# Kernel optimization log

Measured on AMD Instinct MI355X. Metric: run time of the kernel, lower is better.

The kernel has to match this reference:

```python
import math
import jax, jax.numpy as jnp
import numpy as np

B, T, C = 2, 2048, 1024
N_HEAD = 16
HEAD_DIM = C // N_HEAD

def setup_inputs() -> dict:
    key = jax.random.key(0)
    kx, kq, kk, kv, kp = jax.random.split(key, 5)
    s = 1.0 / math.sqrt(C)
    return {
        "x": jax.random.normal(kx, (B, T, C), dtype=jnp.float32),
        "Wq": jax.random.normal(kq, (C, C), dtype=jnp.float32) * s,
        "Wk": jax.random.normal(kk, (C, C), dtype=jnp.float32) * s,
        "Wv": jax.random.normal(kv, (C, C), dtype=jnp.float32) * s,
        "Wproj": jax.random.normal(kp, (C, C), dtype=jnp.float32) * s,
    }

def reference(x, Wq, Wk, Wv, Wproj):
    b, t, c = x.shape
    # nn.Linear(no bias): x @ W.T ; weights stored [out, in]
    def heads(w):
        return (x @ w.T).reshape(b, t, N_HEAD, HEAD_DIM).transpose(0, 2, 1, 3)  # [B,H,T,D]
    q, k, v = heads(Wq), heads(Wk), heads(Wv)
    att = jnp.einsum('bhqd,bhkd->bhqk', q, k) / math.sqrt(HEAD_DIM)  # [B,H,T,T]
    causal = jnp.tril(jnp.ones((t, t), dtype=bool))
    att = jnp.where(causal, att, -jnp.inf)
    att = jax.nn.softmax(att, axis=-1)
    y = jnp.einsum('bhqk,bhkd->bhqd', att, v)           # [B,H,T,D]
    y = y.transpose(0, 2, 1, 3).reshape(b, t, c)        # [B,T,C]
    return y @ Wproj.T
```

## Files before the change

### kernel.cpp

```cpp
#include <hip/hip_runtime.h>
#include <stdint.h>

typedef uint16_t u16;
typedef uint32_t u32;
typedef __attribute__((ext_vector_type(8))) _Float16 f16x8;
typedef __attribute__((ext_vector_type(4))) float f32x4;
typedef __attribute__((ext_vector_type(2))) uint32_t u32x2;

#define NB 2
#define NT 2048
#define NC 1024
#define NH 16
#define ND 64
#define NM (NB*NT)
#define LOG2E 1.44269504088896340736f
#define PSTRIDE 4608

__device__ __forceinline__ u16 f2h(float f) {
  _Float16 h = (_Float16)f;
  return __builtin_bit_cast(u16, h);
}

__global__ __launch_bounds__(256) void cvt_kernel(const float* __restrict__ src,
                                                  u16* __restrict__ dst, int n4) {
  int i = blockIdx.x * 256 + threadIdx.x;
  if (i >= n4) return;
  float4 v = ((const float4*)src)[i];
  ushort4 o;
  o.x = f2h(v.x); o.y = f2h(v.y); o.z = f2h(v.z); o.w = f2h(v.w);
  ((ushort4*)dst)[i] = o;
}

__global__ __launch_bounds__(256) void cvtw_kernel(const float* __restrict__ w0,
                                                   const float* __restrict__ w1,
                                                   const float* __restrict__ w2,
                                                   const float* __restrict__ w3,
                                                   u16* __restrict__ dst) {
  int i = blockIdx.x * 256 + threadIdx.x;
  int which = i >> 18;
  const float* src = (which == 0) ? w0 : (which == 1) ? w1 : (which == 2) ? w2 : w3;
  int j = i & 262143;
  float4 v = ((const float4*)src)[j];
  ushort4 o;
  o.x = f2h(v.x); o.y = f2h(v.y); o.z = f2h(v.z); o.w = f2h(v.w);
  ((ushort4*)dst)[i] = o;
}

__device__ __forceinline__ void gload16(const void* g, void* l) {
  __builtin_amdgcn_global_load_lds(
      (const __attribute__((address_space(1))) void*)g,
      (__attribute__((address_space(3))) void*)l, 16, 0, 0);
}

template<int EPI>
__global__ __launch_bounds__(256) void gemm_bt(const u16* __restrict__ A,
                                               const u16* __restrict__ Bw,
                                               int K, int N,
                                               u16* __restrict__ oq, u16* __restrict__ okk,
                                               u16* __restrict__ ovt,
                                               float* __restrict__ of) {
  __shared__ __align__(16) u16 SH[4*128*64];
  u16* Al = SH;
  u16* Bl = SH + 2*128*64;
  const int tid = threadIdx.x, lane = tid & 63, wid = tid >> 6;
  const int g = lane >> 4, qq = lane & 15;
  const int wm = wid >> 1, wn = wid & 1;
  const int m0 = blockIdx.y * 128, n0 = blockIdx.x * 128;
  const int srow = lane >> 3;
  const int scol8 = (lane & 7) ^ srow;

  f32x4 acc[4][4] = {};
  const int nk = K >> 6;

  #pragma unroll
  for (int pp = 0; pp < 4; ++pp) {
    int r = wid*32 + pp*8;
    gload16(A  + (size_t)(m0 + r + srow)*K + scol8*8, &Al[r*64]);
    gload16(Bw + (size_t)(n0 + r + srow)*K + scol8*8, &Bl[r*64]);
  }

  for (int kt = 0; kt < nk; ++kt) {
    const int cur = kt & 1;
    __syncthreads();
    if (kt + 1 < nk) {
      const int k1 = (kt + 1) << 6;
      #pragma unroll
      for (int pp = 0; pp < 4; ++pp) {
        int r = wid*32 + pp*8;
        gload16(A  + (size_t)(m0 + r + srow)*K + k1 + scol8*8, &Al[(cur^1)*8192 + r*64]);
        gload16(Bw + (size_t)(n0 + r + srow)*K + k1 + scol8*8, &Bl[(cur^1)*8192 + r*64]);
      }
    }
    #pragma unroll
    for (int kk = 0; kk < 2; ++kk) {
      f16x8 af[4], bfr[4];
      #pragma unroll
      for (int mt = 0; mt < 4; ++mt) {
        int row = wm*64 + mt*16 + qq;
        af[mt] = *(const f16x8*)&Al[cur*8192 + row*64 + (((kk*4 + g) ^ (qq & 7))*8)];
      }
      #pragma unroll
      for (int nt = 0; nt < 4; ++nt) {
        int row = wn*64 + nt*16 + qq;
        bfr[nt] = *(const f16x8*)&Bl[cur*8192 + row*64 + (((kk*4 + g) ^ (qq & 7))*8)];
      }
      #pragma unroll
      for (int mt = 0; mt < 4; ++mt)
        #pragma unroll
        for (int nt = 0; nt < 4; ++nt)
          acc[mt][nt] = __builtin_amdgcn_mfma_f32_16x16x32_f16(af[mt], bfr[nt], acc[mt][nt], 0, 0, 0);
    }
  }

  if (EPI == 0) {
    __syncthreads();
    u16* reg = SH + wid*4096;
    const int sel = n0 >> 10;
    const int h = ((n0 & 1023) >> 6) + wn;
    const int bq = m0 >> 11;

    if (sel < 2) {
      const float scale = (sel == 0) ? 0.125f*LOG2E : 1.0f;
      #pragma unroll
      for (int mt = 0; mt < 4; ++mt)
        #pragma unroll
        for (int r = 0; r < 4; ++r) {
          int mloc = mt*16 + g*4 + r;
          #pragma unroll
          for (int nt = 0; nt < 4; ++nt) {
            int d = nt*16 + qq;
            reg[mloc*64 + (d ^ (g << 4))] = f2h(acc[mt][nt][r] * scale);
          }
        }
      u16* dst = (sel == 0) ? oq : okk;
      const int slot = lane & 7;
      #pragma unroll
      for (int i = 0; i < 8; ++i) {
        int row = i*8 + (lane >> 3);
        int physslot = slot ^ (((row >> 2) & 3) << 1);
        f16x8 vvv = *(const f16x8*)&reg[row*64 + physslot*8];
        int m = m0 + wm*64 + row;
        int t = m & (NT-1);
        *(f16x8*)(dst + (((size_t)(bq*NH + h)*NT + t)*ND) + slot*8) = vvv;
      }
    } else {
      #pragma unroll
      for (int nt = 0; nt < 4; ++nt) {
        int d = nt*16 + qq;
        int f = (d & 7) << 3;
        #pragma unroll
        for (int mt = 0; mt < 4; ++mt)
          #pragma unroll
          for (int rp = 0; rp < 2; ++rp) {
            int r = rp*2;
            int mloc = mt*16 + g*4 + r;
            u32 pk = (u32)f2h(acc[mt][nt][r]) | ((u32)f2h(acc[mt][nt][r+1]) << 16);
            *(u32*)&reg[d*64 + (mloc ^ f)] = pk;
          }
      }
      const int slot = lane & 7;
      const int t0 = m0 + wm*64;
      #pragma unroll
      for (int i = 0; i < 8; ++i) {
        int d = i*8 + (lane >> 3);
        int physslot = slot ^ (d & 7);
        f16x8 vvv = *(const f16x8*)&reg[d*64 + physslot*8];
        int t = (t0 & (NT-1)) + slot*8;
        *(f16x8*)(ovt + ((size_t)(bq*NH + h)*ND + d)*NT + t) = vvv;
      }
    }
  } else {
    #pragma unroll
    for (int mt = 0; mt < 4; ++mt)
      #pragma unroll
      for (int r = 0; r < 4; ++r) {
        int m = m0 + wm*64 + mt*16 + g*4 + r;
        #pragma unroll
        for (int nt = 0; nt < 4; ++nt) {
          int n = n0 + wn*64 + nt*16 + qq;
          of[(size_t)m*N + n] = acc[mt][nt][r];
        }
      }
  }
}

#define IT(q,s,c,m) ((u32)(q) | ((u32)(s)<<8) | ((u32)(c)<<16) | ((u32)(m)<<24))
__global__ __launch_bounds__(256) void attn_kernel(const u16* __restrict__ q,
                                                   const u16* __restrict__ k,
                                                   const u16* __restrict__ vt,
                                                   u16* __restrict__ y,
                                                   u16* __restrict__ part) {
  static const u32 items[48] = {
    IT(15,0,16,0), IT(30,0,16,1), IT(31,0,16,1), IT(31,16,16,2),
    IT(14,0,15,0), IT(28,0,15,1), IT(29,0,15,1), IT(29,15,15,2), IT(30,16,15,2),
    IT(13,0,14,0), IT(26,0,14,1), IT(27,0,14,1), IT(27,14,14,2), IT(28,15,14,2),
    IT(12,0,13,0), IT(24,0,13,1), IT(25,0,13,1), IT(25,13,13,2), IT(26,14,13,2),
    IT(11,0,12,0), IT(22,0,12,1), IT(23,0,12,1), IT(23,12,12,2), IT(24,13,12,2),
    IT(10,0,11,0), IT(20,0,11,1), IT(21,0,11,1), IT(21,11,11,2), IT(22,12,11,2),
    IT( 9,0,10,0), IT(18,0,10,1), IT(19,0,10,1), IT(19,10,10,2), IT(20,11,10,2),
    IT( 8,0, 9,0), IT(16,0, 9,1), IT(17,0, 9,1), IT(17, 9, 9,2), IT(18,10, 9,2),
    IT( 7,0, 8,0), IT(16,9, 8,2),
    IT( 6,0, 7,0), IT( 5,0, 6,0), IT( 4,0, 5,0), IT( 3,0, 4,0),
    IT( 2,0, 3,0), IT( 1,0, 2,0), IT( 0,0, 1,0)
  };
  __shared__ __align__(16) u16 Kl[2][64*64];
  __shared__ __align__(16) u16 Vl[2][64*64];
  __shared__ __align__(16) u16 Pl[4*16*64];
  const int tid = threadIdx.x, lane = tid & 63, wid = tid >> 6;
  const int g = lane >> 4, qq = lane & 15;
  const int bh = blockIdx.x;
  const u32 it = items[blockIdx.y];
  const int qtile = it & 255;
  const int ks = (it >> 8) & 255;
  const int kc = (it >> 16) & 255;
  const int mode = it >> 24;
  const int qs = qtile * 64;
  const u16* qp = q  + (size_t)bh*NT*ND;
  const u16* kp = k  + (size_t)bh*NT*ND;
  const u16* vp = vt + (size_t)bh*ND*NT;
  const int b = bh >> 4, h = bh & 15;
  const int srow = lane >> 3;
  const int scol8 = (lane & 7) ^ (srow & 7);
  u16* pl = &Pl[wid*1024];
  u32* plw = (u32*)pl;

  f16x8 aq[2];
  {
    int t = qs + wid*16 + qq;
    #pragma unroll
    for (int c = 0; c < 2; ++c)
      aq[c] = *(const f16x8*)(qp + (size_t)t*ND + c*32 + 8*g);
  }

  f16x8 vones;
  #pragma unroll
  for (int i = 0; i < 8; ++i) vones[i] = (_Float16)1.0f;

  f32x4 accO[4] = {};
  f32x4 accS = {};
  float m_run = -1e30f;

  #pragma unroll
  for (int pp = 0; pp < 2; ++pp) {
    int issue = wid*2 + pp;
    int row = issue*8 + srow;
    gload16(kp + (size_t)(ks*64 + row)*ND + scol8*8, &Kl[0][issue*512]);
    gload16(vp + (size_t)row*NT + ks*64 + scol8*8, &Vl[0][issue*512]);
  }

  for (int kt = ks; kt < ks + kc; ++kt) {
    const int kvs = kt*64;
    const int cur = (kt - ks) & 1;
    __syncthreads();

    if (kt + 1 < ks + kc) {
      const int kvs2 = kvs + 64;
      #pragma unroll
      for (int pp = 0; pp < 2; ++pp) {
        int issue = wid*2 + pp;
        int row = issue*8 + srow;
        gload16(kp + (size_t)(kvs2 + row)*ND + scol8*8, &Kl[cur^1][issue*512]);
        gload16(vp + (size_t)row*NT + kvs2 + scol8*8, &Vl[cur^1][issue*512]);
      }
    }

    f32x4 sacc[4] = {};
    __builtin_amdgcn_s_setprio(1);
    #pragma unroll
    for (int c = 0; c < 2; ++c) {
      #pragma unroll
      for (int nt = 0; nt < 4; ++nt) {
        int row = nt*16 + qq;
        int col = (c*32 + 8*g) ^ ((row & 7) << 3);
        f16x8 kb = *(const f16x8*)&Kl[cur][row*64 + col];
        sacc[nt] = __builtin_amdgcn_mfma_f32_16x16x32_f16(kb, aq[c], sacc[nt], 0, 0, 0);
      }
    }
    __builtin_amdgcn_s_setprio(0);

    if (kvs + 63 > qs + wid*16) {
      int qg = qs + wid*16 + qq;
      #pragma unroll
      for (int nt = 0; nt < 4; ++nt)
        #pragma unroll
        for (int r = 0; r < 4; ++r)
          if (kvs + nt*16 + g*4 + r > qg) sacc[nt][r] = -1e30f;
    }

    float m0a = fmaxf(fmaxf(sacc[0][0], sacc[0][1]), fmaxf(sacc[0][2], sacc[0][3]));
    float m1a = fmaxf(fmaxf(sacc[1][0], sacc[1][1]), fmaxf(sacc[1][2], sacc[1][3]));
    float m2a = fmaxf(fmaxf(sacc[2][0], sacc[2][1]), fmaxf(sacc[2][2], sacc[2][3]));
    float m3a = fmaxf(fmaxf(sacc[3][0], sacc[3][1]), fmaxf(sacc[3][2], sacc[3][3]));
    float mloc = fmaxf(fmaxf(m0a, m1a), fmaxf(m2a, m3a));

    const bool defer = __all(mloc <= m_run + 8.f);
    float mnew;
    if (defer) {
      mnew = m_run;
    } else {
      float mf = fmaxf(mloc, __shfl_xor(mloc, 16));
      mf = fmaxf(mf, __shfl_xor(mf, 32));
      mnew = fmaxf(m_run, mf);
      float a = exp2f(m_run - mnew);
      m_run = mnew;
      #pragma unroll
      for (int r = 0; r < 4; ++r) {
        float ar = __shfl(a, (lane & 48) + g*4 + r);
        #pragma unroll
        for (int nt = 0; nt < 4; ++nt) accO[nt][r] *= ar;
        accS[r] *= ar;
      }
    }

    #pragma unroll
    for (int nt = 0; nt < 4; ++nt) {
      float p0 = exp2f(sacc[nt][0] - mnew);
      float p1 = exp2f(sacc[nt][1] - mnew);
      float p2 = exp2f(sacc[nt][2] - mnew);
      float p3 = exp2f(sacc[nt][3] - mnew);
      u32 pk0 = __builtin_bit_cast(u32, __builtin_amdgcn_cvt_pkrtz(p0, p1));
      u32 pk1 = __builtin_bit_cast(u32, __builtin_amdgcn_cvt_pkrtz(p2, p3));
      int kv0 = nt*16 + g*4;
      u32x2 pr; pr.x = pk0; pr.y = pk1;
      *(u32x2*)&plw[(qq*64 + (kv0 ^ ((qq & 7) << 3))) >> 1] = pr;
    }

    __builtin_amdgcn_s_setprio(1);
    #pragma unroll
    for (int c = 0; c < 2; ++c) {
      f16x8 pa = *(const f16x8*)&pl[qq*64 + ((c*32 + 8*g) ^ ((qq & 7) << 3))];
      accS = __builtin_amdgcn_mfma_f32_16x16x32_f16(pa, vones, accS, 0, 0, 0);
      #pragma unroll
      for (int nt = 0; nt < 4; ++nt) {
        int vrow = nt*16 + qq;
        int vcol = (c*32 + 8*g) ^ ((vrow & 7) << 3);
        f16x8 vb = *(const f16x8*)&Vl[cur][vrow*64 + vcol];
        accO[nt] = __builtin_amdgcn_mfma_f32_16x16x32_f16(pa, vb, accO[nt], 0, 0, 0);
      }
    }
    __builtin_amdgcn_s_setprio(0);
  }

  if (mode == 0) {
    #pragma unroll
    for (int r = 0; r < 4; ++r) {
      float invr = 1.0f / accS[r];
      int t = qs + wid*16 + g*4 + r;
      #pragma unroll
      for (int nt = 0; nt < 4; ++nt) {
        int d = nt*16 + qq;
        y[((size_t)(b*NT + t))*NC + h*ND + d] = f2h(accO[nt][r] * invr);
      }
    }
  } else {
    const int slot = ((bh << 4) + (qtile - 16))*2 + (mode - 1);
    u16* pp = part + (size_t)slot * PSTRIDE;
    float* hd = (float*)(pp + 4096);
    #pragma unroll
    for (int r = 0; r < 4; ++r) {
      int rloc = wid*16 + g*4 + r;
      float l = accS[r];
      float invr = 1.0f / l;
      float mr = __shfl(m_run, (lane & 48) + g*4 + r);
      #pragma unroll
      for (int nt = 0; nt < 4; ++nt) {
        int d = nt*16 + qq;
        pp[rloc*64 + d] = f2h(accO[nt][r] * invr);
      }
      if (qq == 0) { hd[rloc] = mr; hd[64 + rloc] = l; }
    }
  }
}

__global__ __launch_bounds__(256) void combine_kernel(const u16* __restrict__ part,
                                                      u16* __restrict__ y) {
  const int jj = blockIdx.x;
  const int bh = blockIdx.y;
  const int b = bh >> 4, h = bh & 15;
  const u16* p0 = part + (size_t)(((bh << 4) + jj)*2) * PSTRIDE;
  const u16* p1 = p0 + PSTRIDE;
  const float* h0 = (const float*)(p0 + 4096);
  const float* h1 = (const float*)(p1 + 4096);
  const int tid = threadIdx.x;
  const int d0 = (tid & 7) * 8;
  #pragma unroll
  for (int i = 0; i < 2; ++i) {
    int r = (tid >> 3) + 32*i;
    float m1 = h0[r], l1 = h0[64 + r];
    float m2 = h1[r], l2 = h1[64 + r];
    float mm = fmaxf(m1, m2);
    float w1 = exp2f(m1 - mm) * l1, w2 = exp2f(m2 - mm) * l2;
    float inv = 1.0f / (w1 + w2);
    float a1 = w1 * inv, a2 = w2 * inv;
    f16x8 o1 = *(const f16x8*)&p0[r*64 + d0];
    f16x8 o2 = *(const f16x8*)&p1[r*64 + d0];
    f16x8 out;
    #pragma unroll
    for (int e = 0; e < 8; ++e)
      out[e] = (_Float16)(a1 * (float)o1[e] + a2 * (float)o2[e]);
    int t = (16 + jj)*64 + r;
    *(f16x8*)(y + ((size_t)(b*NT + t))*NC + h*ND + d0) = out;
  }
}

extern "C" void kernel_launch(void* const* d_in, const int* in_sizes, int n_in,
                              void* d_out, int out_size, void* d_ws, size_t ws_size,
                              hipStream_t stream) {
  const float* x  = (const float*)d_in[0];
  const float* Wq = (const float*)d_in[1];
  const float* Wk = (const float*)d_in[2];
  const float* Wv = (const float*)d_in[3];
  const float* Wp = (const float*)d_in[4];

  u16* xb   = (u16*)d_ws;
  u16* wqkv = xb   + (size_t)NM*NC;
  u16* wpj  = wqkv + (size_t)3*NC*NC;
  u16* qb   = wpj  + (size_t)NC*NC;
  u16* kb   = qb   + (size_t)NM*NC;
  u16* vtb  = kb   + (size_t)NM*NC;
  u16* yb   = vtb  + (size_t)NM*NC;
  u16* part = xb;
  size_t need = ((size_t)NM*NC*5 + (size_t)4*NC*NC) * sizeof(u16);
  if (ws_size < need) return;

  cvt_kernel<<<NM*NC/4/256, 256, 0, stream>>>(x, xb, NM*NC/4);
  cvtw_kernel<<<4*NC*NC/4/256, 256, 0, stream>>>(Wq, Wk, Wv, Wp, wqkv);

  gemm_bt<0><<<dim3(3*NC/128, NM/128), 256, 0, stream>>>(xb, wqkv, NC, 3*NC,
                                                         qb, kb, vtb, nullptr);
  attn_kernel<<<dim3(NB*NH, 48), 256, 0, stream>>>(qb, kb, vtb, yb, part);
  combine_kernel<<<dim3(16, NB*NH), 256, 0, stream>>>(part, yb);
  gemm_bt<1><<<dim3(NC/128, NM/128), 256, 0, stream>>>(yb, wpj, NC, NC,
                                                       nullptr, nullptr, nullptr,
                                                       (float*)d_out);
}
```

Before: 113.0 us.

## Keep attention P in registers via transposed 16x16x16 MFMA for PV

```diff
diff --git a/kernel.cpp b/kernel.cpp
--- a/kernel.cpp
+++ b/kernel.cpp
@@ -4,6 +4,7 @@
 typedef uint16_t u16;
 typedef uint32_t u32;
 typedef __attribute__((ext_vector_type(8))) _Float16 f16x8;
+typedef __attribute__((ext_vector_type(4))) _Float16 f16x4;
 typedef __attribute__((ext_vector_type(4))) float f32x4;
 typedef __attribute__((ext_vector_type(2))) uint32_t u32x2;
 
@@ -185,11 +186,11 @@
 }
 
 #define IT(q,s,c,m) ((u32)(q) | ((u32)(s)<<8) | ((u32)(c)<<16) | ((u32)(m)<<24))
-__global__ __launch_bounds__(256) void attn_kernel(const u16* __restrict__ q,
-                                                   const u16* __restrict__ k,
-                                                   const u16* __restrict__ vt,
-                                                   u16* __restrict__ y,
-                                                   u16* __restrict__ part) {
+__global__ __launch_bounds__(256, 5) void attn_kernel(const u16* __restrict__ q,
+                                                      const u16* __restrict__ k,
+                                                      const u16* __restrict__ vt,
+                                                      u16* __restrict__ y,
+                                                      u16* __restrict__ part) {
   static const u32 items[48] = {
     IT(15,0,16,0), IT(30,0,16,1), IT(31,0,16,1), IT(31,16,16,2),
     IT(14,0,15,0), IT(28,0,15,1), IT(29,0,15,1), IT(29,15,15,2), IT(30,16,15,2),
@@ -205,7 +206,6 @@
   };
   __shared__ __align__(16) u16 Kl[2][64*64];
   __shared__ __align__(16) u16 Vl[2][64*64];
-  __shared__ __align__(16) u16 Pl[4*16*64];
   const int tid = threadIdx.x, lane = tid & 63, wid = tid >> 6;
   const int g = lane >> 4, qq = lane & 15;
   const int bh = blockIdx.x;
@@ -221,8 +221,6 @@
   const int b = bh >> 4, h = bh & 15;
   const int srow = lane >> 3;
   const int scol8 = (lane & 7) ^ (srow & 7);
-  u16* pl = &Pl[wid*1024];
-  u32* plw = (u32*)pl;
 
   f16x8 aq[2];
   {
@@ -232,9 +230,9 @@
       aq[c] = *(const f16x8*)(qp + (size_t)t*ND + c*32 + 8*g);
   }
 
-  f16x8 vones;
+  f16x4 ones4;
   #pragma unroll
-  for (int i = 0; i < 8; ++i) vones[i] = (_Float16)1.0f;
+  for (int i = 0; i < 4; ++i) ones4[i] = (_Float16)1.0f;
 
   f32x4 accO[4] = {};
   f32x4 accS = {};
@@ -304,71 +302,61 @@
       float a = exp2f(m_run - mnew);
       m_run = mnew;
       #pragma unroll
-      for (int r = 0; r < 4; ++r) {
-        float ar = __shfl(a, (lane & 48) + g*4 + r);
-        #pragma unroll
-        for (int nt = 0; nt < 4; ++nt) accO[nt][r] *= ar;
-        accS[r] *= ar;
-      }
-    }
-
+      for (int dt = 0; dt < 4; ++dt) accO[dt] *= a;
+      accS *= a;
+    }
+
+    f16x4 pb[4];
     #pragma unroll
     for (int nt = 0; nt < 4; ++nt) {
       float p0 = exp2f(sacc[nt][0] - mnew);
       float p1 = exp2f(sacc[nt][1] - mnew);
       float p2 = exp2f(sacc[nt][2] - mnew);
       float p3 = exp2f(sacc[nt][3] - mnew);
-      u32 pk0 = __builtin_bit_cast(u32, __builtin_amdgcn_cvt_pkrtz(p0, p1));
-      u32 pk1 = __builtin_bit_cast(u32, __builtin_amdgcn_cvt_pkrtz(p2, p3));
-      int kv0 = nt*16 + g*4;
-      u32x2 pr; pr.x = pk0; pr.y = pk1;
-      *(u32x2*)&plw[(qq*64 + (kv0 ^ ((qq & 7) << 3))) >> 1] = pr;
+      u32x2 w;
+      w.x = __builtin_bit_cast(u32, __builtin_amdgcn_cvt_pkrtz(p0, p1));
+      w.y = __builtin_bit_cast(u32, __builtin_amdgcn_cvt_pkrtz(p2, p3));
+      pb[nt] = __builtin_bit_cast(f16x4, w);
     }
 
     __builtin_amdgcn_s_setprio(1);
     #pragma unroll
-    for (int c = 0; c < 2; ++c) {
-      f16x8 pa = *(const f16x8*)&pl[qq*64 + ((c*32 + 8*g) ^ ((qq & 7) << 3))];
-      accS = __builtin_amdgcn_mfma_f32_16x16x32_f16(pa, vones, accS, 0, 0, 0);
-      #pragma unroll
-      for (int nt = 0; nt < 4; ++nt) {
-        int vrow = nt*16 + qq;
-        int vcol = (c*32 + 8*g) ^ ((vrow & 7) << 3);
-        f16x8 vb = *(const f16x8*)&Vl[cur][vrow*64 + vcol];
-        accO[nt] = __builtin_amdgcn_mfma_f32_16x16x32_f16(pa, vb, accO[nt], 0, 0, 0);
+    for (int nt = 0; nt < 4; ++nt) {
+      accS = __builtin_amdgcn_mfma_f32_16x16x16f16(ones4, pb[nt], accS, 0, 0, 0);
+      #pragma unroll
+      for (int dt = 0; dt < 4; ++dt) {
+        int vrow = dt*16 + qq;
+        int slot = (2*nt + (g >> 1)) ^ (vrow & 7);
+        f16x4 vb = *(const f16x4*)&Vl[cur][vrow*64 + slot*8 + (g & 1)*4];
+        accO[dt] = __builtin_amdgcn_mfma_f32_16x16x16f16(vb, pb[nt], accO[dt], 0, 0, 0);
       }
     }
     __builtin_amdgcn_s_setprio(0);
   }
 
+  const float inv = 1.0f / accS[0];
   if (mode == 0) {
-    #pragma unroll
-    for (int r = 0; r < 4; ++r) {
-      float invr = 1.0f / accS[r];
-      int t = qs + wid*16 + g*4 + r;
-      #pragma unroll
-      for (int nt = 0; nt < 4; ++nt) {
-        int d = nt*16 + qq;
-        y[((size_t)(b*NT + t))*NC + h*ND + d] = f2h(accO[nt][r] * invr);
-      }
+    int t = qs + wid*16 + qq;
+    #pragma unroll
+    for (int dt = 0; dt < 4; ++dt) {
+      u32x2 st;
+      st.x = (u32)f2h(accO[dt][0]*inv) | ((u32)f2h(accO[dt][1]*inv) << 16);
+      st.y = (u32)f2h(accO[dt][2]*inv) | ((u32)f2h(accO[dt][3]*inv) << 16);
+      *(u32x2*)(y + ((size_t)(b*NT + t))*NC + h*ND + dt*16 + g*4) = st;
     }
   } else {
     const int slot = ((bh << 4) + (qtile - 16))*2 + (mode - 1);
     u16* pp = part + (size_t)slot * PSTRIDE;
     float* hd = (float*)(pp + 4096);
-    #pragma unroll
-    for (int r = 0; r < 4; ++r) {
-      int rloc = wid*16 + g*4 + r;
-      float l = accS[r];
-      float invr = 1.0f / l;
-      float mr = __shfl(m_run, (lane & 48) + g*4 + r);
-      #pragma unroll
-      for (int nt = 0; nt < 4; ++nt) {
-        int d = nt*16 + qq;
-        pp[rloc*64 + d] = f2h(accO[nt][r] * invr);
-      }
-      if (qq == 0) { hd[rloc] = mr; hd[64 + rloc] = l; }
-    }
+    const int rloc = wid*16 + qq;
+    #pragma unroll
+    for (int dt = 0; dt < 4; ++dt) {
+      u32x2 st;
+      st.x = (u32)f2h(accO[dt][0]*inv) | ((u32)f2h(accO[dt][1]*inv) << 16);
+      st.y = (u32)f2h(accO[dt][2]*inv) | ((u32)f2h(accO[dt][3]*inv) << 16);
+      *(u32x2*)(pp + rloc*64 + dt*16 + g*4) = st;
+    }
+    if (g == 0) { hd[rloc] = m_run; hd[64 + rloc] = accS[0]; }
   }
 }
 
```

New measurement: 113.7 us. Within noise of the previous version (+0.6%).
